# Performance work log

Hardware: AMD Instinct MI355X
Metric: run time of the kernel (lower is better)

## Reference

```python
import jax, jax.numpy as jnp
import numpy as np

EMBED_DIM = 512
NUM_HEADS = 8
HEAD_DIM = EMBED_DIM // NUM_HEADS
LN_EPS = 1e-5


def setup_inputs() -> dict:
    key = jax.random.key(0)
    ks = jax.random.split(key, 14)
    B, Lq, Lkv, E = 4, 1024, 4096, EMBED_DIM
    s = 0.02
    return {
        "query": jax.random.normal(ks[0], (B, Lq, E), dtype=jnp.float32),
        "key_value": jax.random.normal(ks[1], (B, Lkv, E), dtype=jnp.float32),
        "w_q": jax.random.normal(ks[2], (E, E), dtype=jnp.float32) * s,
        "w_k": jax.random.normal(ks[3], (E, E), dtype=jnp.float32) * s,
        "w_v": jax.random.normal(ks[4], (E, E), dtype=jnp.float32) * s,
        "b_q": jnp.zeros((E,), dtype=jnp.float32),
        "b_k": jnp.zeros((E,), dtype=jnp.float32),
        "b_v": jnp.zeros((E,), dtype=jnp.float32),
        "w_o": jax.random.normal(ks[5], (E, E), dtype=jnp.float32) * s,
        "b_o": jnp.zeros((E,), dtype=jnp.float32),
        "ln_gamma": jnp.ones((E,), dtype=jnp.float32),
        "ln_beta": jnp.zeros((E,), dtype=jnp.float32),
    }


def reference(query, key_value, w_q, w_k, w_v, b_q, b_k, b_v, w_o, b_o, ln_gamma, ln_beta):
    # query: [B, Lq, E]; key_value: [B, Lkv, E]
    B, Lq, E = query.shape
    Lkv = key_value.shape[1]
    H, D = NUM_HEADS, HEAD_DIM

    q = (query @ w_q.T + b_q).reshape(B, Lq, H, D)
    k = (key_value @ w_k.T + b_k).reshape(B, Lkv, H, D)
    v = (key_value @ w_v.T + b_v).reshape(B, Lkv, H, D)

    scale = 1.0 / jnp.sqrt(jnp.asarray(D, dtype=query.dtype))
    scores = jnp.einsum("bqhd,bkhd->bhqk", q, k) * scale  # [B,H,Lq,Lkv]
    attn = jax.nn.softmax(scores, axis=-1)
    # attn dropout off (eval mode)

    ctx = jnp.einsum("bhqk,bkhd->bqhd", attn, v).reshape(B, Lq, E)
    attn_output = ctx @ w_o.T + b_o
    # post-attn dropout off (eval mode)

    x = query + attn_output
    mu = jnp.mean(x, axis=-1, keepdims=True)
    var = jnp.mean(jnp.square(x - mu), axis=-1, keepdims=True)
    out = (x - mu) / jnp.sqrt(var + LN_EPS) * ln_gamma + ln_beta

    # need_weights=True: PyTorch averages attention weights over heads
    attn_weights = jnp.mean(attn, axis=1)  # [B, Lq, Lkv]
    return out, attn_weights
```

## Files before the change

### kernel.cpp

```cpp
#include <hip/hip_runtime.h>
#include <hip/hip_bf16.h>

namespace {

constexpr int E_DIM = 512;
constexpr int NH = 8;
constexpr int HD = 64;
constexpr int LQ = 1024;
constexpr int LKV = 4096;
constexpr int NB = 4;
constexpr int SPLIT = 4;
constexpr int SLICE = LKV / SPLIT;
constexpr int NT = SLICE / 64;
constexpr int SSPLIT = 8;
constexpr size_t CPL = (size_t)NB * LQ * E_DIM;

typedef __attribute__((ext_vector_type(8))) short bf16x8;
typedef __attribute__((ext_vector_type(8))) unsigned short u16x8;
typedef __attribute__((ext_vector_type(4))) float f32x4;

typedef const unsigned int __attribute__((address_space(1)))* gptr1;
typedef unsigned int __attribute__((address_space(3)))* lptr3;

__device__ __forceinline__ void gl16(const unsigned short* g, unsigned short* l) {
  __builtin_amdgcn_global_load_lds((gptr1)g, (lptr3)l, 16, 0, 0);
}

__device__ __forceinline__ f32x4 mfma16(bf16x8 a, bf16x8 b, f32x4 c) {
  return __builtin_amdgcn_mfma_f32_16x16x32_bf16(a, b, c, 0, 0, 0);
}

__device__ __forceinline__ unsigned short f2b(float f) {
  unsigned int u = __float_as_uint(f);
  u += 0x7FFFu + ((u >> 16) & 1u);
  return (unsigned short)(u >> 16);
}

__device__ __forceinline__ unsigned int cvt_pk_bf16(float a, float b) {
  unsigned int r;
  asm("v_cvt_pk_bf16_f32 %0, %1, %2" : "=v"(r) : "v"(a), "v"(b));
  return r;
}

__global__ __launch_bounds__(256) void cvt_all(
    const float* __restrict__ query, const float* __restrict__ kv,
    const float* __restrict__ w0, const float* __restrict__ w1,
    const float* __restrict__ w2, const float* __restrict__ w3,
    unsigned short* __restrict__ Qxb, unsigned short* __restrict__ KVb,
    unsigned short* __restrict__ Wb) {
  const int blk = blockIdx.x;
  const float* s;
  unsigned short* d;
  size_t idx;
  if (blk < 1024) {
    idx = ((size_t)blk * 256 + threadIdx.x) * 8;
    s = query; d = Qxb;
  } else if (blk < 5120) {
    idx = ((size_t)(blk - 1024) * 256 + threadIdx.x) * 8;
    s = kv; d = KVb;
  } else {
    idx = ((size_t)(blk - 5120) * 256 + threadIdx.x) * 8;
    const int widx = (int)(idx >> 18);
    s = widx == 0 ? w0 : widx == 1 ? w1 : widx == 2 ? w2 : w3;
    d = Wb;
    s -= (size_t)widx << 18;
  }
  const float4 a = *(const float4*)(s + idx);
  const float4 b = *(const float4*)(s + idx + 4);
  uint4 o;
  o.x = cvt_pk_bf16(a.x, a.y);
  o.y = cvt_pk_bf16(a.z, a.w);
  o.z = cvt_pk_bf16(b.x, b.y);
  o.w = cvt_pk_bf16(b.z, b.w);
  *(uint4*)(d + idx) = o;
}

template <int EPI>
__global__ __launch_bounds__(256) void gemm_bf16(
    const unsigned short* __restrict__ A, const unsigned short* __restrict__ B,
    const float* __restrict__ bias, void* __restrict__ outp, int L,
    float oscale) {
  __shared__ __align__(16) unsigned short As[128][32];
  __shared__ __align__(16) unsigned short Bs[128][32];
  const int tid = threadIdx.x;
  const int wv = tid >> 6, lane = tid & 63, lg = lane >> 4, lr = lane & 15;
  const int gx = gridDim.x, gy = gridDim.y;
  const int p = blockIdx.x + gx * blockIdx.y;
  const int xcd = p & 7, ii = p >> 3;
  const int by = xcd * (gy >> 3) + ii / gx;
  const int bx = ii - (ii / gx) * gx;
  const int i0 = by * 128, j0 = bx * 128;
  const int wm = wv >> 1, wn = wv & 1;
  const int srow = tid >> 2, scol = (tid & 3) * 8;
  f32x4 acc[4][4] = {};
  const unsigned short* ap = A + (size_t)(i0 + srow) * E_DIM + scol;
  const unsigned short* bp = B + (size_t)(j0 + srow) * E_DIM + scol;
  unsigned short* lA = &As[srow][scol];
  unsigned short* lB = &Bs[srow][scol];
  for (int k0 = 0; k0 < E_DIM; k0 += 32) {
    __syncthreads();
    gl16(ap + k0, lA);
    gl16(ap + k0 + (size_t)64 * E_DIM, lA + 64 * 32);
    gl16(bp + k0, lB);
    gl16(bp + k0 + (size_t)64 * E_DIM, lB + 64 * 32);
    __syncthreads();
    bf16x8 af[4], bg[4];
    for (int m = 0; m < 4; ++m)
      af[m] = *(const bf16x8*)&As[wm * 64 + m * 16 + lr][lg * 8];
    for (int n = 0; n < 4; ++n)
      bg[n] = *(const bf16x8*)&Bs[wn * 64 + n * 16 + lr][lg * 8];
    for (int m = 0; m < 4; ++m)
      for (int n = 0; n < 4; ++n)
        acc[m][n] = mfma16(af[m], bg[n], acc[m][n]);
  }
  for (int m = 0; m < 4; ++m)
    for (int n = 0; n < 4; ++n) {
      const int j = j0 + wn * 64 + n * 16 + lr;
      const float bj = bias[j];
      for (int r = 0; r < 4; ++r) {
        const int i = i0 + wm * 64 + m * 16 + lg * 4 + r;
        const float v = (acc[m][n][r] + bj) * oscale;
        if (EPI == 2) {
          ((float*)outp)[(size_t)i * E_DIM + j] = v;
        } else {
          const int bb = i / L, li = i - bb * L;
          const int hh = j >> 6, dd = j & 63;
          if (EPI == 0)
            ((unsigned short*)outp)[((size_t)(bb * NH + hh) * L + li) * HD + dd] = f2b(v);
          else
            ((unsigned short*)outp)[((size_t)(bb * NH + hh) * HD + dd) * L + li] = f2b(v);
        }
      }
    }
}

__global__ __launch_bounds__(512, 2) void attn_sums(
    const unsigned short* __restrict__ Qb, const unsigned short* __restrict__ Kb,
    float* __restrict__ l_part) {
  const int tid = threadIdx.x;
  const int h = tid >> 6, lane = tid & 63, lg = lane >> 4, lr = lane & 15;
  const int p = blockIdx.x + 16 * blockIdx.y + 64 * blockIdx.z;
  const int xcd = p & 7, ii = p >> 3;
  const int combo = xcd * 4 + (ii >> 4);
  const int q0 = (ii & 15) * 64;
  const int b = combo >> 3, sp = combo & 7;
  const size_t bh = (size_t)b * NH + h;
  const unsigned short* Qp = Qb + (bh * LQ + q0) * HD;
  const unsigned short* Kp = Kb + (bh * LKV + sp * (LKV / SSPLIT)) * HD;
  bf16x8 qB[4][2];
  for (int qs = 0; qs < 4; ++qs)
    for (int kk = 0; kk < 2; ++kk)
      qB[qs][kk] = *(const bf16x8*)(Qp + (qs * 16 + lr) * HD + kk * 32 + lg * 8);
  float qsum[4] = {};
  for (int t = 0; t < (LKV / SSPLIT) / 64; ++t) {
    const unsigned short* base = Kp + (size_t)t * 64 * HD;
    for (int k2h = 0; k2h < 2; ++k2h) {
      bf16x8 kA[2][2];
      for (int k2 = 0; k2 < 2; ++k2)
        for (int kk = 0; kk < 2; ++kk)
          kA[k2][kk] = *(const bf16x8*)(base + ((k2h * 2 + k2) * 16 + lr) * HD +
                                        kk * 32 + lg * 8);
      f32x4 sacc[2][4] = {};
      for (int k2 = 0; k2 < 2; ++k2)
        for (int qs = 0; qs < 4; ++qs)
          sacc[k2][qs] = mfma16(kA[k2][1], qB[qs][1],
                                mfma16(kA[k2][0], qB[qs][0], sacc[k2][qs]));
      for (int k2 = 0; k2 < 2; ++k2)
        for (int qs = 0; qs < 4; ++qs)
          for (int r = 0; r < 4; ++r)
            qsum[qs] += __builtin_amdgcn_exp2f(sacc[k2][qs][r]);
    }
  }
  for (int qs = 0; qs < 4; ++qs) {
    float v = qsum[qs];
    v += __shfl_xor(v, 16);
    v += __shfl_xor(v, 32);
    if (lg == 0)
      l_part[(size_t)sp * (NB * NH * LQ) + bh * LQ + q0 + qs * 16 + lr] = v;
  }
}

__global__ __launch_bounds__(512) void attn_main(
    const unsigned short* __restrict__ Qb, const unsigned short* __restrict__ Kb,
    const unsigned short* __restrict__ Vt, const float* __restrict__ l_part,
    float* __restrict__ attn_w, unsigned short* __restrict__ ctxp) {
  __shared__ __align__(16) unsigned short P[2][NH][64][64];
  const int tid = threadIdx.x;
  const int h = tid >> 6, lane = tid & 63, lg = lane >> 4, lr = lane & 15;
  const int p = blockIdx.x + 16 * blockIdx.y + 64 * blockIdx.z;
  const int xcd = p & 7, ii = p >> 3;
  const int combo = xcd * 2 + (ii >> 4);
  const int q0 = (ii & 15) * 64;
  const int b = combo >> 2, sp = combo & 3;
  const size_t bh = (size_t)b * NH + h;
  const unsigned short* Qp = Qb + (bh * LQ + q0) * HD;
  const unsigned short* Kp = Kb + (bh * LKV + sp * SLICE) * HD;
  const unsigned short* Vp = Vt + bh * HD * LKV + sp * SLICE;

  bf16x8 qB[4][2];
  for (int qs = 0; qs < 4; ++qs)
    for (int kk = 0; kk < 2; ++kk)
      qB[qs][kk] = *(const bf16x8*)(Qp + (qs * 16 + lr) * HD + kk * 32 + lg * 8);
  float nlg[4];
  for (int qs = 0; qs < 4; ++qs) {
    float ls = 0.f;
    for (int s = 0; s < SSPLIT; ++s)
      ls += l_part[(size_t)s * (NB * NH * LQ) + bh * LQ + q0 + qs * 16 + lr];
    nlg[qs] = -__builtin_amdgcn_logf(ls) - 3.0f;
  }

  f32x4 cacc[4][4] = {};
  for (int t = 0; t < NT; ++t) {
    const int kv0 = t * 64;
    unsigned short (*Pb)[64][64] = P[t & 1];
    bf16x8 vf[4][2];
    for (int ds = 0; ds < 4; ++ds)
      for (int kk = 0; kk < 2; ++kk)
        vf[ds][kk] = *(const bf16x8*)(Vp + (size_t)(ds * 16 + lr) * LKV + kv0 +
                                      kk * 32 + lg * 8);
    for (int kh = 0; kh < 2; ++kh) {
      bf16x8 kA[2][2];
      for (int k2 = 0; k2 < 2; ++k2)
        for (int kk = 0; kk < 2; ++kk)
          kA[k2][kk] = *(const bf16x8*)(Kp + (size_t)(kv0 + (kh * 2 + k2) * 16 + lr) * HD +
                                        kk * 32 + lg * 8);
      f32x4 sacc[2][4] = {};
      for (int k2 = 0; k2 < 2; ++k2)
        for (int qs = 0; qs < 4; ++qs)
          sacc[k2][qs] = mfma16(kA[k2][1], qB[qs][1],
                                mfma16(kA[k2][0], qB[qs][0], sacc[k2][qs]));
      for (int k2 = 0; k2 < 2; ++k2)
        for (int qs = 0; qs < 4; ++qs) {
          const int q = qs * 16 + lr;
          const float p0 = __builtin_amdgcn_exp2f(sacc[k2][qs][0] + nlg[qs]);
          const float p1 = __builtin_amdgcn_exp2f(sacc[k2][qs][1] + nlg[qs]);
          const float p2 = __builtin_amdgcn_exp2f(sacc[k2][qs][2] + nlg[qs]);
          const float p3 = __builtin_amdgcn_exp2f(sacc[k2][qs][3] + nlg[qs]);
          uint2 w;
          w.x = cvt_pk_bf16(p0, p1);
          w.y = cvt_pk_bf16(p2, p3);
          const int col = ((kh * 2 + k2) * 16 + lg * 4) ^ ((q & 7) << 3);
          *(uint2*)&Pb[h][q][col] = w;
        }
    }
    for (int kk = 0; kk < 2; ++kk) {
      bf16x8 pa[4];
      for (int qs = 0; qs < 4; ++qs) {
        const int q = qs * 16 + lr;
        pa[qs] = *(const bf16x8*)&Pb[h][q][(kk * 32 + lg * 8) ^ ((q & 7) << 3)];
      }
      for (int qs = 0; qs < 4; ++qs)
        for (int ds = 0; ds < 4; ++ds)
          cacc[qs][ds] = mfma16(pa[qs], vf[ds][kk], cacc[qs][ds]);
    }
    __syncthreads();
    {
      const int qa = tid >> 3, La = tid & 7;
      const int col = (La * 8) ^ ((qa & 7) << 3);
      float2 s01 = {0.f, 0.f}, s23 = {0.f, 0.f}, s45 = {0.f, 0.f},
             s67 = {0.f, 0.f};
      for (int hh = 0; hh < NH; ++hh) {
        const uint4 v = *(const uint4*)&Pb[hh][qa][col];
        s01.x += __uint_as_float(v.x << 16);
        s01.y += __uint_as_float(v.x & 0xFFFF0000u);
        s23.x += __uint_as_float(v.y << 16);
        s23.y += __uint_as_float(v.y & 0xFFFF0000u);
        s45.x += __uint_as_float(v.z << 16);
        s45.y += __uint_as_float(v.z & 0xFFFF0000u);
        s67.x += __uint_as_float(v.w << 16);
        s67.y += __uint_as_float(v.w & 0xFFFF0000u);
      }
      float* op = attn_w + (size_t)(b * LQ + q0 + qa) * LKV + sp * SLICE + kv0 +
                  La * 8;
      float4 o0 = {s01.x, s01.y, s23.x, s23.y};
      float4 o1 = {s45.x, s45.y, s67.x, s67.y};
      *(float4*)op = o0;
      *(float4*)(op + 4) = o1;
    }
  }
  unsigned short* cp = ctxp + (size_t)sp * CPL;
  for (int qs = 0; qs < 4; ++qs)
    for (int ds = 0; ds < 4; ++ds)
      for (int r = 0; r < 4; ++r)
        cp[(size_t)(b * LQ + q0 + qs * 16 + lg * 4 + r) * E_DIM + h * HD +
           ds * 16 + lr] = f2b(cacc[qs][ds][r]);
}

__global__ __launch_bounds__(256) void combine_ctx(
    const unsigned short* __restrict__ ctxp, unsigned short* __restrict__ ctxb) {
  const size_t i = (size_t)blockIdx.x * 256 + threadIdx.x;
  float2 s01 = {0.f, 0.f}, s23 = {0.f, 0.f}, s45 = {0.f, 0.f}, s67 = {0.f, 0.f};
  for (int pl = 0; pl < SPLIT; ++pl) {
    const uint4 v = ((const uint4*)(ctxp + pl * CPL))[i];
    s01.x += __uint_as_float(v.x << 16);
    s01.y += __uint_as_float(v.x & 0xFFFF0000u);
    s23.x += __uint_as_float(v.y << 16);
    s23.y += __uint_as_float(v.y & 0xFFFF0000u);
    s45.x += __uint_as_float(v.z << 16);
    s45.y += __uint_as_float(v.z & 0xFFFF0000u);
    s67.x += __uint_as_float(v.w << 16);
    s67.y += __uint_as_float(v.w & 0xFFFF0000u);
  }
  uint4 o;
  o.x = cvt_pk_bf16(s01.x, s01.y);
  o.y = cvt_pk_bf16(s23.x, s23.y);
  o.z = cvt_pk_bf16(s45.x, s45.y);
  o.w = cvt_pk_bf16(s67.x, s67.y);
  ((uint4*)ctxb)[i] = o;
}

__global__ __launch_bounds__(256) void ln_kernel(
    const float* __restrict__ q, const float* __restrict__ ao,
    const float* __restrict__ gamma, const float* __restrict__ beta,
    float* __restrict__ out) {
  const int row = blockIdx.x;
  const int tid = threadIdx.x;
  const size_t base = (size_t)row * E_DIM;
  const float x0 = q[base + tid] + ao[base + tid];
  const float x1 = q[base + 256 + tid] + ao[base + 256 + tid];
  float s = x0 + x1, ss = x0 * x0 + x1 * x1;
  for (int off = 32; off >= 1; off >>= 1) {
    s += __shfl_down(s, off);
    ss += __shfl_down(ss, off);
  }
  __shared__ float ps[4], pss[4];
  if ((tid & 63) == 0) {
    ps[tid >> 6] = s;
    pss[tid >> 6] = ss;
  }
  __syncthreads();
  s = ps[0] + ps[1] + ps[2] + ps[3];
  ss = pss[0] + pss[1] + pss[2] + pss[3];
  const float mu = s * (1.f / E_DIM);
  float var = ss * (1.f / E_DIM) - mu * mu;
  var = fmaxf(var, 0.f);
  const float rstd = rsqrtf(var + 1e-5f);
  out[base + tid] = (x0 - mu) * rstd * gamma[tid] + beta[tid];
  out[base + 256 + tid] = (x1 - mu) * rstd * gamma[256 + tid] + beta[256 + tid];
}

}

extern "C" void kernel_launch(void* const* d_in, const int* in_sizes, int n_in,
                              void* d_out, int out_size, void* d_ws, size_t ws_size,
                              hipStream_t stream) {
  const float* query = (const float*)d_in[0];
  const float* key_value = (const float*)d_in[1];
  const float* w_q = (const float*)d_in[2];
  const float* w_k = (const float*)d_in[3];
  const float* w_v = (const float*)d_in[4];
  const float* b_q = (const float*)d_in[5];
  const float* b_k = (const float*)d_in[6];
  const float* b_v = (const float*)d_in[7];
  const float* w_o = (const float*)d_in[8];
  const float* b_o = (const float*)d_in[9];
  const float* ln_g = (const float*)d_in[10];
  const float* ln_b = (const float*)d_in[11];

  unsigned short* Qb = (unsigned short*)d_ws;
  unsigned short* Kb = Qb + (size_t)2097152;
  unsigned short* Vt = Kb + (size_t)8388608;
  float* l_part = (float*)(Vt + (size_t)8388608);
  unsigned short* Wb = (unsigned short*)(l_part + 262144);
  float* ao = (float*)(Wb + 1048576);
  unsigned short* KVb = (unsigned short*)(ao + 2097152);
  unsigned short* Qxb = KVb + (size_t)8388608;
  unsigned short* ctxp = KVb;
  unsigned short* ctxb = Qb;

  float* out = (float*)d_out;
  float* attn_w = out + (size_t)NB * LQ * E_DIM;

  const float qscale = 0.125f * 1.44269504088896340736f;

  cvt_all<<<dim3(5632), dim3(256), 0, stream>>>(query, key_value, w_q, w_k, w_v,
                                                w_o, Qxb, KVb, Wb);

  gemm_bf16<0><<<dim3(4, 32), dim3(256), 0, stream>>>(Qxb, Wb, b_q, Qb, LQ, qscale);
  gemm_bf16<0><<<dim3(4, 128), dim3(256), 0, stream>>>(KVb, Wb + 262144, b_k, Kb,
                                                       LKV, 1.0f);
  gemm_bf16<1><<<dim3(4, 128), dim3(256), 0, stream>>>(KVb, Wb + 524288, b_v, Vt,
                                                       LKV, 8.0f);

  attn_sums<<<dim3(16, NB, SSPLIT), dim3(512), 0, stream>>>(Qb, Kb, l_part);
  attn_main<<<dim3(16, NB, SPLIT), dim3(512), 0, stream>>>(Qb, Kb, Vt, l_part,
                                                           attn_w, ctxp);
  combine_ctx<<<dim3(1024), dim3(256), 0, stream>>>(ctxp, ctxb);
  gemm_bf16<2><<<dim3(4, 32), dim3(256), 0, stream>>>(ctxb, Wb + 786432, b_o, ao,
                                                      LQ, 1.0f);
  ln_kernel<<<dim3(NB * LQ), dim3(256), 0, stream>>>(query, ao, ln_g, ln_b, out);
}
```

Baseline: 251.5 us.

## Fuse softmax-sum and main attention kernels with inter-block flag barrier

Merges the row-sum pass and the main attention pass into one kernel. Each block computes partial exp sums for its KV slice, then waits on an atomic flag until all SPLIT blocks sharing the same batch and query group have published theirs. This removes one kernel launch and reuses the loaded Q fragments, and the sum pass now uses SPLIT=4 blocks instead of 8, which halves its parallelism. The spin-wait depends on all 256 blocks being co-resident and risks deadlock if they are not.

```diff
diff --git a/kernel.cpp b/kernel.cpp
--- a/kernel.cpp
+++ b/kernel.cpp
@@ -12,7 +12,6 @@
 constexpr int SPLIT = 4;
 constexpr int SLICE = LKV / SPLIT;
 constexpr int NT = SLICE / 64;
-constexpr int SSPLIT = 8;
 constexpr size_t CPL = (size_t)NB * LQ * E_DIM;
 
 typedef __attribute__((ext_vector_type(8))) short bf16x8;
@@ -134,25 +133,32 @@
     }
 }
 
-__global__ __launch_bounds__(512, 2) void attn_sums(
+__global__ __launch_bounds__(512) void attn_fused(
     const unsigned short* __restrict__ Qb, const unsigned short* __restrict__ Kb,
-    float* __restrict__ l_part) {
+    const unsigned short* __restrict__ Vt, float* __restrict__ l_part,
+    int* __restrict__ flags, float* __restrict__ attn_w,
+    unsigned short* __restrict__ ctxp) {
+  __shared__ __align__(16) unsigned short P[2][NH][64][64];
   const int tid = threadIdx.x;
   const int h = tid >> 6, lane = tid & 63, lg = lane >> 4, lr = lane & 15;
   const int p = blockIdx.x + 16 * blockIdx.y + 64 * blockIdx.z;
   const int xcd = p & 7, ii = p >> 3;
-  const int combo = xcd * 4 + (ii >> 4);
-  const int q0 = (ii & 15) * 64;
-  const int b = combo >> 3, sp = combo & 7;
+  const int combo = xcd * 2 + (ii >> 4);
+  const int qg = ii & 15;
+  const int q0 = qg * 64;
+  const int b = combo >> 2, sp = combo & 3;
   const size_t bh = (size_t)b * NH + h;
   const unsigned short* Qp = Qb + (bh * LQ + q0) * HD;
-  const unsigned short* Kp = Kb + (bh * LKV + sp * (LKV / SSPLIT)) * HD;
+  const unsigned short* Kp = Kb + (bh * LKV + sp * SLICE) * HD;
+  const unsigned short* Vp = Vt + bh * HD * LKV + sp * SLICE;
+
   bf16x8 qB[4][2];
   for (int qs = 0; qs < 4; ++qs)
     for (int kk = 0; kk < 2; ++kk)
       qB[qs][kk] = *(const bf16x8*)(Qp + (qs * 16 + lr) * HD + kk * 32 + lg * 8);
+
   float qsum[4] = {};
-  for (int t = 0; t < (LKV / SSPLIT) / 64; ++t) {
+  for (int t = 0; t < NT; ++t) {
     const unsigned short* base = Kp + (size_t)t * 64 * HD;
     for (int k2h = 0; k2h < 2; ++k2h) {
       bf16x8 kA[2][2];
@@ -178,33 +184,21 @@
     if (lg == 0)
       l_part[(size_t)sp * (NB * NH * LQ) + bh * LQ + q0 + qs * 16 + lr] = v;
   }
-}
-
-__global__ __launch_bounds__(512) void attn_main(
-    const unsigned short* __restrict__ Qb, const unsigned short* __restrict__ Kb,
-    const unsigned short* __restrict__ Vt, const float* __restrict__ l_part,
-    float* __restrict__ attn_w, unsigned short* __restrict__ ctxp) {
-  __shared__ __align__(16) unsigned short P[2][NH][64][64];
-  const int tid = threadIdx.x;
-  const int h = tid >> 6, lane = tid & 63, lg = lane >> 4, lr = lane & 15;
-  const int p = blockIdx.x + 16 * blockIdx.y + 64 * blockIdx.z;
-  const int xcd = p & 7, ii = p >> 3;
-  const int combo = xcd * 2 + (ii >> 4);
-  const int q0 = (ii & 15) * 64;
-  const int b = combo >> 2, sp = combo & 3;
-  const size_t bh = (size_t)b * NH + h;
-  const unsigned short* Qp = Qb + (bh * LQ + q0) * HD;
-  const unsigned short* Kp = Kb + (bh * LKV + sp * SLICE) * HD;
-  const unsigned short* Vp = Vt + bh * HD * LKV + sp * SLICE;
-
-  bf16x8 qB[4][2];
-  for (int qs = 0; qs < 4; ++qs)
-    for (int kk = 0; kk < 2; ++kk)
-      qB[qs][kk] = *(const bf16x8*)(Qp + (qs * 16 + lr) * HD + kk * 32 + lg * 8);
+  __syncthreads();
+  if (tid == 0) {
+    __threadfence();
+    int* fl = &flags[b * 16 + qg];
+    __hip_atomic_fetch_add(fl, 1, __ATOMIC_ACQ_REL, __HIP_MEMORY_SCOPE_AGENT);
+    while (__hip_atomic_load(fl, __ATOMIC_ACQUIRE, __HIP_MEMORY_SCOPE_AGENT) < SPLIT) {
+    }
+    __threadfence();
+  }
+  __syncthreads();
+
   float nlg[4];
   for (int qs = 0; qs < 4; ++qs) {
     float ls = 0.f;
-    for (int s = 0; s < SSPLIT; ++s)
+    for (int s = 0; s < SPLIT; ++s)
       ls += l_part[(size_t)s * (NB * NH * LQ) + bh * LQ + q0 + qs * 16 + lr];
     nlg[qs] = -__builtin_amdgcn_logf(ls) - 3.0f;
   }
@@ -361,6 +355,7 @@
   unsigned short* Kb = Qb + (size_t)2097152;
   unsigned short* Vt = Kb + (size_t)8388608;
   float* l_part = (float*)(Vt + (size_t)8388608);
+  int* flags = (int*)(l_part + (size_t)SPLIT * NB * NH * LQ);
   unsigned short* Wb = (unsigned short*)(l_part + 262144);
   float* ao = (float*)(Wb + 1048576);
   unsigned short* KVb = (unsigned short*)(ao + 2097152);
@@ -373,6 +368,8 @@
 
   const float qscale = 0.125f * 1.44269504088896340736f;
 
+  hipMemsetAsync(flags, 0, sizeof(int) * NB * 16, stream);
+
   cvt_all<<<dim3(5632), dim3(256), 0, stream>>>(query, key_value, w_q, w_k, w_v,
                                                 w_o, Qxb, KVb, Wb);
 
@@ -382,9 +379,8 @@
   gemm_bf16<1><<<dim3(4, 128), dim3(256), 0, stream>>>(KVb, Wb + 524288, b_v, Vt,
                                                        LKV, 8.0f);
 
-  attn_sums<<<dim3(16, NB, SSPLIT), dim3(512), 0, stream>>>(Qb, Kb, l_part);
-  attn_main<<<dim3(16, NB, SPLIT), dim3(512), 0, stream>>>(Qb, Kb, Vt, l_part,
-                                                           attn_w, ctxp);
+  attn_fused<<<dim3(16, NB, SPLIT), dim3(512), 0, stream>>>(Qb, Kb, Vt, l_part,
+                                                            flags, attn_w, ctxp);
   combine_ctx<<<dim3(1024), dim3(256), 0, stream>>>(ctxp, ctxb);
   gemm_bf16<2><<<dim3(4, 32), dim3(256), 0, stream>>>(ctxb, Wb + 786432, b_o, ao,
                                                       LQ, 1.0f);
```

Measured after the change: 219.3 us. -12.8%, faster.
